# Optimization experiments

Hardware: AMD Instinct MI355X
Metric: run time of the kernel (lower is better)

Reference implementation:

```python
import jax, jax.numpy as jnp
import numpy as np

N = 10000      # nodes
E = 160000     # edges
IN = 256       # input feature dim
HID = 128      # hidden per head
H = 4          # heads (all layers)
EMB = 128      # dim_embedding (last-layer out per head)
SLOPE = 0.2    # leaky_relu negative slope in attention


def _gat_layer(h, src, dst, W, al, ar, b, residual, apply_act):
    """DGL-style GATConv (no dropout). h: [N, F_in], W: [F_in, H*D], al/ar/b: [H, D]."""
    n = h.shape[0]
    heads, d = al.shape
    feat = (h @ W).reshape(n, heads, d)                 # [N, H, D]
    el = jnp.sum(feat * al, axis=-1)                    # [N, H]
    er = jnp.sum(feat * ar, axis=-1)                    # [N, H]
    e = jax.nn.leaky_relu(el[src] + er[dst], SLOPE)     # [E, H]
    # edge softmax over incoming edges of dst (numerically stable)
    m = jax.ops.segment_max(e, dst, num_segments=n)
    m = jnp.where(jnp.isfinite(m), m, 0.0)              # empty segments -> 0
    ex = jnp.exp(e - m[dst])
    den = jax.ops.segment_sum(ex, dst, num_segments=n)
    alpha = ex / jnp.maximum(den[dst], 1e-9)            # [E, H]
    rst = jax.ops.segment_sum(alpha[:, :, None] * feat[src], dst, num_segments=n)  # [N, H, D]
    if residual:
        rst = rst + h.reshape(n, heads, d)              # identity residual (dims match)
    rst = rst + b
    return jax.nn.elu(rst) if apply_act else rst


def setup_inputs() -> dict:
    key = jax.random.key(0)
    ks = jax.random.split(key, 24)
    def p(k, shape, scale):
        return (jax.random.normal(k, shape, jnp.float32) * scale)
    inp = {
        'x': jax.random.normal(ks[0], (N, IN), jnp.float32),
        'src': jax.random.randint(ks[1], (E,), 0, N, dtype=jnp.int32).astype(jnp.int64),
        'dst': jax.random.randint(ks[2], (E,), 0, N, dtype=jnp.int32).astype(jnp.int64),
        # layer 0: in=IN, out=HID per head
        'W0': p(ks[3], (IN, H * HID), 1.0 / np.sqrt(IN)),
        'al0': p(ks[4], (H, HID), 0.1), 'ar0': p(ks[5], (H, HID), 0.1),
        'b0': p(ks[6], (H, HID), 0.02),
        # layer 1: in=H*HID=512, out=HID per head, residual
        'W1': p(ks[7], (H * HID, H * HID), 1.0 / np.sqrt(H * HID)),
        'al1': p(ks[8], (H, HID), 0.1), 'ar1': p(ks[9], (H, HID), 0.1),
        'b1': p(ks[10], (H, HID), 0.02),
        # layer 2: in=H*HID=512, out=EMB per head, residual, no activation
        'W2': p(ks[11], (H * HID, H * EMB), 1.0 / np.sqrt(H * HID)),
        'al2': p(ks[12], (H, EMB), 0.1), 'ar2': p(ks[13], (H, EMB), 0.1),
        'b2': p(ks[14], (H, EMB), 0.02),
        # MLP predictor: 2*EMB -> EMB -> EMB//2 -> 1
        'Wm0': p(ks[15], (2 * EMB, EMB), 1.0 / np.sqrt(2 * EMB)), 'bm0': p(ks[16], (EMB,), 0.02),
        'Wm1': p(ks[17], (EMB, EMB // 2), 1.0 / np.sqrt(EMB)), 'bm1': p(ks[18], (EMB // 2,), 0.02),
        'Wm2': p(ks[19], (EMB // 2, 1), 1.0 / np.sqrt(EMB // 2)), 'bm2': p(ks[20], (1,), 0.02),
    }
    return inp


def reference(x, src, dst, W0, al0, ar0, b0, W1, al1, ar1, b1, W2, al2, ar2, b2,
              Wm0, bm0, Wm1, bm1, Wm2, bm2):
    # GAT encoder
    h = _gat_layer(x, src, dst, W0, al0, ar0, b0, residual=False, apply_act=True).reshape(N, -1)
    h = _gat_layer(h, src, dst, W1, al1, ar1, b1, residual=True, apply_act=True).reshape(N, -1)
    h = _gat_layer(h, src, dst, W2, al2, ar2, b2, residual=True, apply_act=False).mean(axis=1)  # [N, EMB]
    # link predictor over all graph edges
    emb = jnp.concatenate([h[src], h[dst]], axis=1)     # [E, 2*EMB]
    z = jax.nn.relu(emb @ Wm0 + bm0)
    z = jax.nn.relu(z @ Wm1 + bm1)
    return jax.nn.sigmoid(z @ Wm2 + bm2)                # [E, 1]
```

## Files before the change

### kernel.cpp

```cpp
#include <hip/hip_runtime.h>
#include <hip/hip_bf16.h>
#include <math.h>

constexpr int kN = 10000;
constexpr int kE = 160000;
constexpr float kSlope = 0.2f;

typedef short v8s __attribute__((ext_vector_type(8)));
typedef float f32x4 __attribute__((ext_vector_type(4)));
typedef unsigned short ushort_t;

__device__ __forceinline__ float lrelu(float x) { return x > 0.f ? x : kSlope * x; }
__device__ __forceinline__ float elu_f(float x) { return x > 0.f ? x : (expf(x) - 1.f); }
__device__ __forceinline__ float b2f(ushort_t u) {
    return __uint_as_float(((unsigned)u) << 16);
}
__device__ __forceinline__ ushort_t f2b(float f) {
    unsigned u = __float_as_uint(f);
    return (ushort_t)((u + 0x7FFFu + ((u >> 16) & 1u)) >> 16);
}

__global__ void detect_zero(const void* __restrict__ x, const void* __restrict__ dsti,
                            int* __restrict__ flags, int* __restrict__ deg) {
    if (blockIdx.x == 0) {
        __shared__ int sb[2];
        int tid = threadIdx.x;
        if (tid == 0) { sb[0] = 0; sb[1] = 0; }
        __syncthreads();
        const ushort_t* xb = (const ushort_t*)x;
        int big = 0;
        for (int i = tid; i < 4096; i += 256) {
            float v = b2f(xb[i]);
            if (!(fabsf(v) <= 1e4f)) big = 1;
        }
        const int* d32 = (const int*)dsti;
        int hi = 0;
        for (int i = tid; i < 4096; i += 256) hi |= d32[2 * i + 1];
        if (big) atomicOr(&sb[0], 1);
        if (hi)  atomicOr(&sb[1], 1);
        __syncthreads();
        if (tid == 0) { flags[0] = sb[0]; flags[1] = sb[1] ? 0 : 1; }
    } else {
        int i = (blockIdx.x - 1) * 256 + threadIdx.x;
        if (i < 2 * kN) deg[i] = 0;
    }
}

struct PrepArgs {
    const void* sm[13];
    const void* W0; const void* W1; const void* W2; const void* Wm0; const void* Wm1;
    const void* X; const void* srcIn; const void* dstIn;
    float* smallb;
    ushort_t* W0T; ushort_t* W1T; ushort_t* W2T; ushort_t* PQT; ushort_t* Wm1T;
    ushort_t* Xb;
    int* nsrc; int* ndst; int* deg;
    const int* flags;
};
constexpr int kPrepTotal = 4865 + 131072 + 262144 + 262144 + 32768 + 8192 + 2560000 + 320000;

__global__ void prep_all(PrepArgs a) {
    int i = blockIdx.x * 256 + threadIdx.x;
    if (i >= kPrepTotal) return;
    const int f32in = a.flags[0];
    auto cv = [&](const void* p, int idx) -> ushort_t {
        return f32in ? f2b(((const float*)p)[idx]) : ((const ushort_t*)p)[idx];
    };
    if (i < 4865) {
        int seg, offi;
        if (i < 4608)      { seg = i >> 9; offi = i & 511; }
        else if (i < 4736) { seg = 9;  offi = i - 4608; }
        else if (i < 4800) { seg = 10; offi = i - 4736; }
        else if (i < 4864) { seg = 11; offi = i - 4800; }
        else               { seg = 12; offi = 0; }
        a.smallb[i] = f32in ? ((const float*)a.sm[seg])[offi]
                            : b2f(((const ushort_t*)a.sm[seg])[offi]);
        return;
    }
    i -= 4865;
    if (i < 131072) {
        int n = i >> 8, k = i & 255;
        a.W0T[i] = cv(a.W0, k * 512 + n);
        return;
    }
    i -= 131072;
    if (i < 262144) {
        int n = i >> 9, k = i & 511;
        a.W1T[i] = cv(a.W1, k * 512 + n);
        return;
    }
    i -= 262144;
    if (i < 262144) {
        int n = i >> 9, k = i & 511;
        a.W2T[i] = cv(a.W2, k * 512 + n);
        return;
    }
    i -= 262144;
    if (i < 32768) {
        int n = i >> 7, k = i & 127;
        a.PQT[i] = cv(a.Wm0, (k + ((n < 128) ? 0 : 128)) * 128 + (n & 127));
        return;
    }
    i -= 32768;
    if (i < 8192) {
        int n = i >> 7, k = i & 127;
        a.Wm1T[i] = cv(a.Wm1, k * 64 + n);
        return;
    }
    i -= 8192;
    if (i < 2560000) {
        if (f32in) a.Xb[i] = f2b(((const float*)a.X)[i]);
        return;
    }
    i -= 2560000;
    {
        const void* in = (i < kE) ? a.srcIn : a.dstIn;
        int j = (i < kE) ? i : i - kE;
        int v = a.flags[1] ? (int)((const long long*)in)[j] : ((const int*)in)[j];
        v = ((unsigned)v < (unsigned)kN) ? v : 0;
        if (i < kE) a.nsrc[j] = v;
        else { a.ndst[j] = v; atomicAdd(&a.deg[v], 1); }
    }
}

__global__ __launch_bounds__(1024) void scan_off(const int* __restrict__ deg,
                                                 int* __restrict__ off, int n) {
    __shared__ int s[1024];
    int tid = threadIdx.x;
    int per = (n + 1023) >> 10;
    int base = tid * per;
    int sum = 0;
    for (int i = 0; i < per; ++i) { int j = base + i; if (j < n) sum += deg[j]; }
    s[tid] = sum;
    __syncthreads();
    for (int d = 1; d < 1024; d <<= 1) {
        int v = (tid >= d) ? s[tid - d] : 0;
        __syncthreads();
        s[tid] += v;
        __syncthreads();
    }
    int run = (tid > 0) ? s[tid - 1] : 0;
    for (int i = 0; i < per; ++i) {
        int j = base + i;
        if (j < n) { off[j] = run; run += deg[j]; }
    }
    if (tid == 0) off[n] = s[1023];
}

__global__ void fill_csr(const int* __restrict__ src, const int* __restrict__ dst,
                         const int* __restrict__ off, int* __restrict__ cnt,
                         int* __restrict__ ss, int* __restrict__ eid,
                         int* __restrict__ dpos, int n) {
    int i = blockIdx.x * 256 + threadIdx.x;
    if (i < n) {
        int d = dst[i];
        int pos = off[d] + atomicAdd(&cnt[d], 1);
        if (pos < kE) { ss[pos] = src[i]; eid[pos] = i; dpos[pos] = d; }
    }
}

template <bool ELER>
__global__ __launch_bounds__(256) void gemm_mfma(const ushort_t* __restrict__ A,
                                                 const void* __restrict__ Araw,
                                                 const int* __restrict__ gflags,
                                                 const ushort_t* __restrict__ WT,
                                                 ushort_t* __restrict__ Cout,
                                                 int M, int N, int K,
                                                 const float* __restrict__ al,
                                                 const float* __restrict__ ar,
                                                 float* __restrict__ el,
                                                 float* __restrict__ er) {
    __shared__ __align__(16) ushort_t As[4][64][8];
    __shared__ __align__(16) ushort_t Bs[4][128][8];
    __shared__ float elred[64][2][2];
    const int t = threadIdx.x;
    const int wave = t >> 6, lane = t & 63;
    const int l16 = lane & 15, q = lane >> 4;
    const int row0 = blockIdx.y * 64, col0 = blockIdx.x * 128;
    const int wm = (wave & 1) * 32, wn = (wave >> 1) * 64;
    const int am = t >> 2, ak8 = t & 3;
    const int sw = ak8 * 4;

    const ushort_t* Aeff = A;
    if (Araw != nullptr && gflags[0] == 0) Aeff = (const ushort_t*)Araw;

    const ushort_t* aptr = Aeff + (size_t)min(row0 + am, M - 1) * K + ak8 * 8;
    const ushort_t* bptr0 = WT + (size_t)(col0 + am) * K + ak8 * 8;
    const ushort_t* bptr1 = bptr0 + (size_t)64 * K;

    uint4 ga  = *(const uint4*)aptr;
    uint4 gb0 = *(const uint4*)bptr0;
    uint4 gb1 = *(const uint4*)bptr1;

    f32x4 acc[2][4];
#pragma unroll
    for (int mt = 0; mt < 2; ++mt)
#pragma unroll
        for (int nt = 0; nt < 4; ++nt)
#pragma unroll
            for (int r = 0; r < 4; ++r) acc[mt][nt][r] = 0.f;

    for (int k0 = 0; k0 < K; k0 += 32) {
        __syncthreads();
        *(uint4*)&As[ak8][am ^ sw][0] = ga;
        *(uint4*)&Bs[ak8][am ^ sw][0] = gb0;
        *(uint4*)&Bs[ak8][(am + 64) ^ sw][0] = gb1;
        __syncthreads();
        if (k0 + 32 < K) {
            ga  = *(const uint4*)(aptr + k0 + 32);
            gb0 = *(const uint4*)(bptr0 + k0 + 32);
            gb1 = *(const uint4*)(bptr1 + k0 + 32);
        }
        v8s af[2], bf[4];
        const int qs = q * 4;
#pragma unroll
        for (int mt = 0; mt < 2; ++mt)
            af[mt] = *(const v8s*)&As[q][(wm + mt * 16 + l16) ^ qs][0];
#pragma unroll
        for (int nt = 0; nt < 4; ++nt)
            bf[nt] = *(const v8s*)&Bs[q][(wn + nt * 16 + l16) ^ qs][0];
#pragma unroll
        for (int mt = 0; mt < 2; ++mt)
#pragma unroll
            for (int nt = 0; nt < 4; ++nt)
                acc[mt][nt] = __builtin_amdgcn_mfma_f32_16x16x32_bf16(af[mt], bf[nt],
                                                                      acc[mt][nt], 0, 0, 0);
    }
#pragma unroll
    for (int mt = 0; mt < 2; ++mt)
#pragma unroll
        for (int r = 0; r < 4; ++r) {
            int row = row0 + wm + mt * 16 + q * 4 + r;
            if (row < M) {
#pragma unroll
                for (int nt = 0; nt < 4; ++nt)
                    Cout[(size_t)row * N + col0 + wn + nt * 16 + l16] = f2b(acc[mt][nt][r]);
            }
        }
    if (ELER) {
        const int head = blockIdx.x;
        float alv[4], arv[4];
#pragma unroll
        for (int nt = 0; nt < 4; ++nt) {
            alv[nt] = al[head * 128 + wn + nt * 16 + l16];
            arv[nt] = ar[head * 128 + wn + nt * 16 + l16];
        }
#pragma unroll
        for (int mt = 0; mt < 2; ++mt)
#pragma unroll
            for (int r = 0; r < 4; ++r) {
                float pel = 0.f, per = 0.f;
#pragma unroll
                for (int nt = 0; nt < 4; ++nt) {
                    pel += acc[mt][nt][r] * alv[nt];
                    per += acc[mt][nt][r] * arv[nt];
                }
                pel += __shfl_xor(pel, 1); per += __shfl_xor(per, 1);
                pel += __shfl_xor(pel, 2); per += __shfl_xor(per, 2);
                pel += __shfl_xor(pel, 4); per += __shfl_xor(per, 4);
                pel += __shfl_xor(pel, 8); per += __shfl_xor(per, 8);
                if (l16 == 0) {
                    int rl = wm + mt * 16 + q * 4 + r;
                    elred[rl][wave >> 1][0] = pel;
                    elred[rl][wave >> 1][1] = per;
                }
            }
        __syncthreads();
        if (t < 64) {
            int row = row0 + t;
            if (row < M) {
                el[row * 4 + head] = elred[t][0][0] + elred[t][1][0];
                er[row * 4 + head] = elred[t][0][1] + elred[t][1][1];
            }
        }
    }
}

template <bool RES, bool ACT, int EPI>
__global__ __launch_bounds__(256) void gat_agg(const ushort_t* __restrict__ feat,
                                               const float* __restrict__ el,
                                               const float* __restrict__ er,
                                               const int* __restrict__ off,
                                               const int* __restrict__ ss,
                                               const ushort_t* residb,
                                               const float* __restrict__ bias,
                                               ushort_t* hl) {
    const int node = blockIdx.x * 4 + (threadIdx.x >> 6);
    const int lane = threadIdx.x & 63;
    if (node >= kN) return;
    const int off0 = off[node];
    const int deg = off[node + 1] - off0;
    float4 er4 = *(const float4*)(er + node * 4);
    const int head = lane >> 4;
    const float erh = (head == 0) ? er4.x : (head == 1) ? er4.y : (head == 2) ? er4.z : er4.w;

    const int c0 = lane * 8;
    float den = 0.f;
    float acc0[8] = {};
    float acc1[8] = {};
    if (deg > 0) {
        int sA = ss[off0];
        int sB = (deg > 1) ? ss[off0 + 1] : sA;
        float eA = el[sA * 4 + head];
        float eB = el[sB * 4 + head];
        const ushort_t* fA = feat + (size_t)sA * 512 + c0;
        const ushort_t* fB = feat + (size_t)sB * 512 + c0;
        ushort4 a0 = *(const ushort4*)fA, a1 = *(const ushort4*)(fA + 4);
        ushort4 b0 = *(const ushort4*)fB, b1 = *(const ushort4*)(fB + 4);
        for (int j = 0; j < deg; j += 2) {
            int sC = (j + 2 < deg) ? ss[off0 + j + 2] : sA;
            int sD = (j + 3 < deg) ? ss[off0 + j + 3] : sA;
            float eC = el[sC * 4 + head];
            float eD = el[sD * 4 + head];
            const ushort_t* fC = feat + (size_t)sC * 512 + c0;
            const ushort_t* fD = feat + (size_t)sD * 512 + c0;
            ushort4 c0v = *(const ushort4*)fC, c1v = *(const ushort4*)(fC + 4);
            ushort4 d0v = *(const ushort4*)fD, d1v = *(const ushort4*)(fD + 4);
            {
                float w0 = expf(lrelu(eA + erh));
                den += w0;
                acc0[0] += w0 * b2f(a0.x); acc0[1] += w0 * b2f(a0.y);
                acc0[2] += w0 * b2f(a0.z); acc0[3] += w0 * b2f(a0.w);
                acc0[4] += w0 * b2f(a1.x); acc0[5] += w0 * b2f(a1.y);
                acc0[6] += w0 * b2f(a1.z); acc0[7] += w0 * b2f(a1.w);
            }
            if (j + 1 < deg) {
                float w1 = expf(lrelu(eB + erh));
                den += w1;
                acc1[0] += w1 * b2f(b0.x); acc1[1] += w1 * b2f(b0.y);
                acc1[2] += w1 * b2f(b0.z); acc1[3] += w1 * b2f(b0.w);
                acc1[4] += w1 * b2f(b1.x); acc1[5] += w1 * b2f(b1.y);
                acc1[6] += w1 * b2f(b1.z); acc1[7] += w1 * b2f(b1.w);
            }
            eA = eC; eB = eD;
            a0 = c0v; a1 = c1v; b0 = d0v; b1 = d1v;
        }
    }
    const float inv = 1.f / fmaxf(den, 1e-9f);
    float4 b0 = *(const float4*)(bias + c0);
    float4 b1 = *(const float4*)(bias + c0 + 4);
    float v[8];
#pragma unroll
    for (int r = 0; r < 8; ++r) v[r] = (acc0[r] + acc1[r]) * inv;
    v[0] += b0.x; v[1] += b0.y; v[2] += b0.z; v[3] += b0.w;
    v[4] += b1.x; v[5] += b1.y; v[6] += b1.z; v[7] += b1.w;
    if (RES) {
        const ushort_t* rp = residb + (size_t)node * 512 + c0;
        ushort4 r0 = *(const ushort4*)rp;
        ushort4 r1 = *(const ushort4*)(rp + 4);
        v[0] += b2f(r0.x); v[1] += b2f(r0.y); v[2] += b2f(r0.z); v[3] += b2f(r0.w);
        v[4] += b2f(r1.x); v[5] += b2f(r1.y); v[6] += b2f(r1.z); v[7] += b2f(r1.w);
    }
    if (ACT) {
#pragma unroll
        for (int r = 0; r < 8; ++r) v[r] = elu_f(v[r]);
    }
    if (EPI == 1) {
        ushort_t* hp = hl + (size_t)node * 512 + c0;
        ushort4 h0 = {f2b(v[0]), f2b(v[1]), f2b(v[2]), f2b(v[3])};
        ushort4 h1 = {f2b(v[4]), f2b(v[5]), f2b(v[6]), f2b(v[7])};
        *(ushort4*)hp = h0;
        *(ushort4*)(hp + 4) = h1;
    }
    if (EPI == 2) {
        float m[8];
#pragma unroll
        for (int r = 0; r < 8; ++r) {
            float x = v[r] + __shfl_xor(v[r], 16);
            x += __shfl_xor(x, 32);
            m[r] = 0.25f * x;
        }
        if (lane < 16) {
            ushort_t* hp = hl + (size_t)node * 128 + lane * 8;
            ushort4 h0 = {f2b(m[0]), f2b(m[1]), f2b(m[2]), f2b(m[3])};
            ushort4 h1 = {f2b(m[4]), f2b(m[5]), f2b(m[6]), f2b(m[7])};
            *(ushort4*)hp = h0;
            *(ushort4*)(hp + 4) = h1;
        }
    }
}

__global__ __launch_bounds__(256) void edge_mfma(const ushort_t* __restrict__ PQb,
                                                 const float* __restrict__ bm0f,
                                                 const ushort_t* __restrict__ Wm1T,
                                                 const float* __restrict__ bm1f,
                                                 const float* __restrict__ wm2f,
                                                 const float* __restrict__ bm2f,
                                                 const int* __restrict__ ss,
                                                 const int* __restrict__ dpos,
                                                 const int* __restrict__ eid,
                                                 void* __restrict__ outv,
                                                 const int* __restrict__ flags) {
    const int t = threadIdx.x;
    const int wave = t >> 6, lane = t & 63;
    const int l16 = lane & 15, q = lane >> 4;
    const int base = blockIdx.x * 64 + wave * 16;
    const int pos = base + l16;
    const int s = ss[pos], d = dpos[pos];
    const ushort_t* prow = PQb + (size_t)s * 256;
    const ushort_t* qrow = PQb + (size_t)d * 256 + 128;

    f32x4 acc[4];
#pragma unroll
    for (int nt = 0; nt < 4; ++nt)
#pragma unroll
        for (int r = 0; r < 4; ++r) acc[nt][r] = 0.f;

#pragma unroll
    for (int ks = 0; ks < 4; ++ks) {
        const int k0 = ks * 32 + q * 8;
        ushort4 p0 = *(const ushort4*)(prow + k0);
        ushort4 p1 = *(const ushort4*)(prow + k0 + 4);
        ushort4 q0 = *(const ushort4*)(qrow + k0);
        ushort4 q1 = *(const ushort4*)(qrow + k0 + 4);
        float4 bb0 = *(const float4*)(bm0f + k0);
        float4 bb1 = *(const float4*)(bm0f + k0 + 4);
        v8s a;
        a[0] = (short)f2b(fmaxf(b2f(p0.x) + b2f(q0.x) + bb0.x, 0.f));
        a[1] = (short)f2b(fmaxf(b2f(p0.y) + b2f(q0.y) + bb0.y, 0.f));
        a[2] = (short)f2b(fmaxf(b2f(p0.z) + b2f(q0.z) + bb0.z, 0.f));
        a[3] = (short)f2b(fmaxf(b2f(p0.w) + b2f(q0.w) + bb0.w, 0.f));
        a[4] = (short)f2b(fmaxf(b2f(p1.x) + b2f(q1.x) + bb1.x, 0.f));
        a[5] = (short)f2b(fmaxf(b2f(p1.y) + b2f(q1.y) + bb1.y, 0.f));
        a[6] = (short)f2b(fmaxf(b2f(p1.z) + b2f(q1.z) + bb1.z, 0.f));
        a[7] = (short)f2b(fmaxf(b2f(p1.w) + b2f(q1.w) + bb1.w, 0.f));
#pragma unroll
        for (int nt = 0; nt < 4; ++nt) {
            v8s b = *(const v8s*)(Wm1T + (size_t)(nt * 16 + l16) * 128 + k0);
            acc[nt] = __builtin_amdgcn_mfma_f32_16x16x32_bf16(a, b, acc[nt], 0, 0, 0);
        }
    }
    float b1v[4], w2v[4];
#pragma unroll
    for (int nt = 0; nt < 4; ++nt) {
        b1v[nt] = bm1f[nt * 16 + l16];
        w2v[nt] = wm2f[nt * 16 + l16];
    }
    float b2 = bm2f[0];
    const int f32out = flags[0];
#pragma unroll
    for (int r = 0; r < 4; ++r) {
        float v = 0.f;
#pragma unroll
        for (int nt = 0; nt < 4; ++nt)
            v += fmaxf(acc[nt][r] + b1v[nt], 0.f) * w2v[nt];
        v += __shfl_xor(v, 1);
        v += __shfl_xor(v, 2);
        v += __shfl_xor(v, 4);
        v += __shfl_xor(v, 8);
        if (l16 == 0) {
            int e = eid[base + q * 4 + r];
            float rr = 1.f / (1.f + expf(-(v + b2)));
            if (f32out) ((float*)outv)[e] = rr;
            else        ((ushort_t*)outv)[e] = f2b(rr);
        }
    }
}

extern "C" void kernel_launch(void* const* d_in, const int* in_sizes, int n_in,
                              void* d_out, int out_size, void* d_ws, size_t ws_size,
                              hipStream_t stream) {
    (void)in_sizes; (void)n_in; (void)out_size; (void)ws_size;

    float* w = (float*)d_ws;
    size_t o = 0;
    auto alloc = [&](size_t n) { float* p = w + o; o += (n + 3) & ~size_t(3); return p; };
    float* smallb = alloc(4868);
    float* al0f = smallb + 0;    float* ar0f = smallb + 512;  float* b0f  = smallb + 1024;
    float* al1f = smallb + 1536; float* ar1f = smallb + 2048; float* b1f  = smallb + 2560;
    float* al2f = smallb + 3072; float* ar2f = smallb + 3584; float* b2f_ = smallb + 4096;
    float* bm0f = smallb + 4608; float* bm1f = smallb + 4736;
    float* wm2f = smallb + 4800; float* bm2f = smallb + 4864;
    float* elb  = alloc((size_t)kN * 4);
    float* erb  = alloc((size_t)kN * 4);
    ushort_t* Fb  = (ushort_t*)alloc((size_t)kN * 256);
    ushort_t* AHL = (ushort_t*)alloc((size_t)kN * 256);
    ushort_t* MHb = (ushort_t*)alloc((size_t)kN * 64);
    ushort_t* Xb  = (ushort_t*)alloc((size_t)kN * 128);
    ushort_t* W0T  = (ushort_t*)alloc(65536);
    ushort_t* W1T  = (ushort_t*)alloc(131072);
    ushort_t* W2T  = (ushort_t*)alloc(131072);
    ushort_t* PQT  = (ushort_t*)alloc(16384);
    ushort_t* Wm1T = (ushort_t*)alloc(4096);
    int* ip    = (int*)(w + o);
    int* flags = ip;
    int* deg   = ip + 4;
    int* cnt   = deg + kN;
    int* off   = cnt + kN;
    int* ss    = off + 10004;
    int* eid   = ss + kE;
    int* dpos  = eid + kE;
    int* nsrc  = dpos + kE;
    int* ndst  = nsrc + kE;

    ushort_t* PQb = Fb;

    dim3 blk(256);

    detect_zero<<<dim3(1 + (2 * kN + 255) / 256), blk, 0, stream>>>(d_in[0], d_in[2], flags, deg);

    PrepArgs a;
    const int sidx[13] = {4, 5, 6, 8, 9, 10, 12, 13, 14, 16, 18, 19, 20};
    for (int i = 0; i < 13; ++i) a.sm[i] = d_in[sidx[i]];
    a.W0 = d_in[3]; a.W1 = d_in[7]; a.W2 = d_in[11]; a.Wm0 = d_in[15]; a.Wm1 = d_in[17];
    a.X = d_in[0]; a.srcIn = d_in[1]; a.dstIn = d_in[2];
    a.smallb = smallb; a.W0T = W0T; a.W1T = W1T; a.W2T = W2T; a.PQT = PQT; a.Wm1T = Wm1T;
    a.Xb = Xb; a.nsrc = nsrc; a.ndst = ndst; a.deg = deg; a.flags = flags;
    prep_all<<<dim3((kPrepTotal + 255) / 256), blk, 0, stream>>>(a);

    scan_off<<<dim3(1), dim3(1024), 0, stream>>>(deg, off, kN);
    fill_csr<<<dim3((kE + 255) / 256), blk, 0, stream>>>(nsrc, ndst, off, cnt, ss, eid, dpos, kE);

    const int gy = (kN + 63) / 64;
    const int ga = (kN + 3) / 4;

    gemm_mfma<true><<<dim3(4, gy), blk, 0, stream>>>(Xb, d_in[0], flags, W0T, Fb,
                                                     kN, 512, 256, al0f, ar0f, elb, erb);
    gat_agg<false, true, 1><<<dim3(ga), blk, 0, stream>>>(Fb, elb, erb, off, ss,
                                                          nullptr, b0f, AHL);

    gemm_mfma<true><<<dim3(4, gy), blk, 0, stream>>>(AHL, nullptr, flags, W1T, Fb,
                                                     kN, 512, 512, al1f, ar1f, elb, erb);
    gat_agg<true, true, 1><<<dim3(ga), blk, 0, stream>>>(Fb, elb, erb, off, ss,
                                                         AHL, b1f, AHL);

    gemm_mfma<true><<<dim3(4, gy), blk, 0, stream>>>(AHL, nullptr, flags, W2T, Fb,
                                                     kN, 512, 512, al2f, ar2f, elb, erb);
    gat_agg<true, false, 2><<<dim3(ga), blk, 0, stream>>>(Fb, elb, erb, off, ss,
                                                          AHL, b2f_, MHb);

    gemm_mfma<false><<<dim3(2, gy), blk, 0, stream>>>(MHb, nullptr, flags, PQT, PQb,
                                                      kN, 256, 128,
                                                      nullptr, nullptr, nullptr, nullptr);

    edge_mfma<<<dim3(kE / 64), blk, 0, stream>>>(PQb, bm0f, Wm1T, bm1f, wm2f, bm2f,
                                                 ss, dpos, eid, d_out, flags);
}
```

Baseline: 326.0 us.

## Double-buffer GEMM via direct global-to-LDS loads and deepen aggregation prefetch

The GEMM now stages tiles with global_load_lds directly into a double-buffered shared-memory layout. This removes the register round trip and one barrier per K step, so loads for the next tile overlap with MFMA work. The aggregation kernel prefetches four neighbours at a time using 16-byte loads and single accumulators, and uses fast __expf. The link-predictor loads are widened to uint4. The risks are a possible LDS swizzle or layout mismatch with the direct-to-LDS writes, and fast-math exp precision differences.

```diff
diff --git a/kernel.cpp b/kernel.cpp
--- a/kernel.cpp
+++ b/kernel.cpp
@@ -11,13 +11,20 @@
 typedef unsigned short ushort_t;
 
 __device__ __forceinline__ float lrelu(float x) { return x > 0.f ? x : kSlope * x; }
-__device__ __forceinline__ float elu_f(float x) { return x > 0.f ? x : (expf(x) - 1.f); }
+__device__ __forceinline__ float elu_f(float x) { return x > 0.f ? x : (__expf(x) - 1.f); }
 __device__ __forceinline__ float b2f(ushort_t u) {
     return __uint_as_float(((unsigned)u) << 16);
 }
+__device__ __forceinline__ float bl(unsigned u) { return __uint_as_float(u << 16); }
+__device__ __forceinline__ float bh(unsigned u) { return __uint_as_float(u & 0xffff0000u); }
 __device__ __forceinline__ ushort_t f2b(float f) {
     unsigned u = __float_as_uint(f);
     return (ushort_t)((u + 0x7FFFu + ((u >> 16) & 1u)) >> 16);
+}
+__device__ __forceinline__ void gload16(const void* g, void* l) {
+    __builtin_amdgcn_global_load_lds(
+        (const __attribute__((address_space(1))) void*)g,
+        (__attribute__((address_space(3))) void*)l, 16, 0, 0);
 }
 
 __global__ void detect_zero(const void* __restrict__ x, const void* __restrict__ dsti,
@@ -169,27 +176,28 @@
                                                  const float* __restrict__ ar,
                                                  float* __restrict__ el,
                                                  float* __restrict__ er) {
-    __shared__ __align__(16) ushort_t As[4][64][8];
-    __shared__ __align__(16) ushort_t Bs[4][128][8];
+    __shared__ __align__(16) ushort_t As[2][4][64][8];
+    __shared__ __align__(16) ushort_t Bs[2][4][128][8];
     __shared__ float elred[64][2][2];
     const int t = threadIdx.x;
     const int wave = t >> 6, lane = t & 63;
     const int l16 = lane & 15, q = lane >> 4;
     const int row0 = blockIdx.y * 64, col0 = blockIdx.x * 128;
     const int wm = (wave & 1) * 32, wn = (wave >> 1) * 64;
-    const int am = t >> 2, ak8 = t & 3;
-    const int sw = ak8 * 4;
 
     const ushort_t* Aeff = A;
     if (Araw != nullptr && gflags[0] == 0) Aeff = (const ushort_t*)Araw;
 
-    const ushort_t* aptr = Aeff + (size_t)min(row0 + am, M - 1) * K + ak8 * 8;
-    const ushort_t* bptr0 = WT + (size_t)(col0 + am) * K + ak8 * 8;
-    const ushort_t* bptr1 = bptr0 + (size_t)64 * K;
-
-    uint4 ga  = *(const uint4*)aptr;
-    uint4 gb0 = *(const uint4*)bptr0;
-    uint4 gb1 = *(const uint4*)bptr1;
+    const int lsw = lane ^ (wave * 4);
+    const ushort_t* asrc  = Aeff + (size_t)min(row0 + lsw, M - 1) * K + wave * 8;
+    const ushort_t* bsrc0 = WT + (size_t)(col0 + lsw) * K + wave * 8;
+    const ushort_t* bsrc1 = WT + (size_t)(col0 + 64 + lsw) * K + wave * 8;
+
+    auto stage = [&](int b, int k0) {
+        gload16(asrc + k0,  &As[b][wave][0][0]);
+        gload16(bsrc0 + k0, &Bs[b][wave][0][0]);
+        gload16(bsrc1 + k0, &Bs[b][wave][64][0]);
+    };
 
     f32x4 acc[2][4];
 #pragma unroll
@@ -199,32 +207,34 @@
 #pragma unroll
             for (int r = 0; r < 4; ++r) acc[mt][nt][r] = 0.f;
 
-    for (int k0 = 0; k0 < K; k0 += 32) {
-        __syncthreads();
-        *(uint4*)&As[ak8][am ^ sw][0] = ga;
-        *(uint4*)&Bs[ak8][am ^ sw][0] = gb0;
-        *(uint4*)&Bs[ak8][(am + 64) ^ sw][0] = gb1;
-        __syncthreads();
-        if (k0 + 32 < K) {
-            ga  = *(const uint4*)(aptr + k0 + 32);
-            gb0 = *(const uint4*)(bptr0 + k0 + 32);
-            gb1 = *(const uint4*)(bptr1 + k0 + 32);
-        }
+    const int qs = q * 4;
+    auto compute = [&](int b) {
         v8s af[2], bf[4];
-        const int qs = q * 4;
 #pragma unroll
         for (int mt = 0; mt < 2; ++mt)
-            af[mt] = *(const v8s*)&As[q][(wm + mt * 16 + l16) ^ qs][0];
+            af[mt] = *(const v8s*)&As[b][q][(wm + mt * 16 + l16) ^ qs][0];
 #pragma unroll
         for (int nt = 0; nt < 4; ++nt)
-            bf[nt] = *(const v8s*)&Bs[q][(wn + nt * 16 + l16) ^ qs][0];
+            bf[nt] = *(const v8s*)&Bs[b][q][(wn + nt * 16 + l16) ^ qs][0];
 #pragma unroll
         for (int mt = 0; mt < 2; ++mt)
 #pragma unroll
             for (int nt = 0; nt < 4; ++nt)
                 acc[mt][nt] = __builtin_amdgcn_mfma_f32_16x16x32_bf16(af[mt], bf[nt],
                                                                       acc[mt][nt], 0, 0, 0);
-    }
+    };
+
+    stage(0, 0);
+    __syncthreads();
+    for (int k0 = 0; k0 < K; k0 += 64) {
+        stage(1, k0 + 32);
+        compute(0);
+        __syncthreads();
+        if (k0 + 64 < K) stage(0, k0 + 64);
+        compute(1);
+        __syncthreads();
+    }
+
 #pragma unroll
     for (int mt = 0; mt < 2; ++mt)
 #pragma unroll
@@ -292,47 +302,41 @@
     float4 er4 = *(const float4*)(er + node * 4);
     const int head = lane >> 4;
     const float erh = (head == 0) ? er4.x : (head == 1) ? er4.y : (head == 2) ? er4.z : er4.w;
-
     const int c0 = lane * 8;
+
     float den = 0.f;
-    float acc0[8] = {};
-    float acc1[8] = {};
+    float acc[8] = {};
     if (deg > 0) {
-        int sA = ss[off0];
-        int sB = (deg > 1) ? ss[off0 + 1] : sA;
-        float eA = el[sA * 4 + head];
-        float eB = el[sB * 4 + head];
-        const ushort_t* fA = feat + (size_t)sA * 512 + c0;
-        const ushort_t* fB = feat + (size_t)sB * 512 + c0;
-        ushort4 a0 = *(const ushort4*)fA, a1 = *(const ushort4*)(fA + 4);
-        ushort4 b0 = *(const ushort4*)fB, b1 = *(const ushort4*)(fB + 4);
-        for (int j = 0; j < deg; j += 2) {
-            int sC = (j + 2 < deg) ? ss[off0 + j + 2] : sA;
-            int sD = (j + 3 < deg) ? ss[off0 + j + 3] : sA;
-            float eC = el[sC * 4 + head];
-            float eD = el[sD * 4 + head];
-            const ushort_t* fC = feat + (size_t)sC * 512 + c0;
-            const ushort_t* fD = feat + (size_t)sD * 512 + c0;
-            ushort4 c0v = *(const ushort4*)fC, c1v = *(const ushort4*)(fC + 4);
-            ushort4 d0v = *(const ushort4*)fD, d1v = *(const ushort4*)(fD + 4);
-            {
-                float w0 = expf(lrelu(eA + erh));
-                den += w0;
-                acc0[0] += w0 * b2f(a0.x); acc0[1] += w0 * b2f(a0.y);
-                acc0[2] += w0 * b2f(a0.z); acc0[3] += w0 * b2f(a0.w);
-                acc0[4] += w0 * b2f(a1.x); acc0[5] += w0 * b2f(a1.y);
-                acc0[6] += w0 * b2f(a1.z); acc0[7] += w0 * b2f(a1.w);
+        float eP[4]; uint4 fP[4];
+#pragma unroll
+        for (int i = 0; i < 4; ++i) {
+            int s = ss[off0 + min(i, deg - 1)];
+            eP[i] = el[s * 4 + head];
+            fP[i] = *(const uint4*)(feat + (size_t)s * 512 + c0);
+        }
+        for (int j = 0; j < deg; j += 4) {
+            float eN[4]; uint4 fN[4];
+            if (j + 4 < deg) {
+#pragma unroll
+                for (int i = 0; i < 4; ++i) {
+                    int s = ss[off0 + min(j + 4 + i, deg - 1)];
+                    eN[i] = el[s * 4 + head];
+                    fN[i] = *(const uint4*)(feat + (size_t)s * 512 + c0);
+                }
             }
-            if (j + 1 < deg) {
-                float w1 = expf(lrelu(eB + erh));
-                den += w1;
-                acc1[0] += w1 * b2f(b0.x); acc1[1] += w1 * b2f(b0.y);
-                acc1[2] += w1 * b2f(b0.z); acc1[3] += w1 * b2f(b0.w);
-                acc1[4] += w1 * b2f(b1.x); acc1[5] += w1 * b2f(b1.y);
-                acc1[6] += w1 * b2f(b1.z); acc1[7] += w1 * b2f(b1.w);
+#pragma unroll
+            for (int i = 0; i < 4; ++i) {
+                if (j + i < deg) {
+                    float w = __expf(lrelu(eP[i] + erh));
+                    den += w;
+                    acc[0] += w * bl(fP[i].x); acc[1] += w * bh(fP[i].x);
+                    acc[2] += w * bl(fP[i].y); acc[3] += w * bh(fP[i].y);
+                    acc[4] += w * bl(fP[i].z); acc[5] += w * bh(fP[i].z);
+                    acc[6] += w * bl(fP[i].w); acc[7] += w * bh(fP[i].w);
+                }
             }
-            eA = eC; eB = eD;
-            a0 = c0v; a1 = c1v; b0 = d0v; b1 = d1v;
+#pragma unroll
+            for (int i = 0; i < 4; ++i) { eP[i] = eN[i]; fP[i] = fN[i]; }
         }
     }
     const float inv = 1.f / fmaxf(den, 1e-9f);
@@ -340,15 +344,15 @@
     float4 b1 = *(const float4*)(bias + c0 + 4);
     float v[8];
 #pragma unroll
-    for (int r = 0; r < 8; ++r) v[r] = (acc0[r] + acc1[r]) * inv;
+    for (int r = 0; r < 8; ++r) v[r] = acc[r] * inv;
     v[0] += b0.x; v[1] += b0.y; v[2] += b0.z; v[3] += b0.w;
     v[4] += b1.x; v[5] += b1.y; v[6] += b1.z; v[7] += b1.w;
     if (RES) {
-        const ushort_t* rp = residb + (size_t)node * 512 + c0;
-        ushort4 r0 = *(const ushort4*)rp;
-        ushort4 r1 = *(const ushort4*)(rp + 4);
-        v[0] += b2f(r0.x); v[1] += b2f(r0.y); v[2] += b2f(r0.z); v[3] += b2f(r0.w);
-        v[4] += b2f(r1.x); v[5] += b2f(r1.y); v[6] += b2f(r1.z); v[7] += b2f(r1.w);
+        uint4 rv = *(const uint4*)(residb + (size_t)node * 512 + c0);
+        v[0] += bl(rv.x); v[1] += bh(rv.x);
+        v[2] += bl(rv.y); v[3] += bh(rv.y);
+        v[4] += bl(rv.z); v[5] += bh(rv.z);
+        v[6] += bl(rv.w); v[7] += bh(rv.w);
     }
     if (ACT) {
 #pragma unroll
@@ -408,21 +412,19 @@
 #pragma unroll
     for (int ks = 0; ks < 4; ++ks) {
         const int k0 = ks * 32 + q * 8;
-        ushort4 p0 = *(const ushort4*)(prow + k0);
-        ushort4 p1 = *(const ushort4*)(prow + k0 + 4);
-        ushort4 q0 = *(const ushort4*)(qrow + k0);
-        ushort4 q1 = *(const ushort4*)(qrow + k0 + 4);
+        uint4 pv = *(const uint4*)(prow + k0);
+        uint4 qv = *(const uint4*)(qrow + k0);
         float4 bb0 = *(const float4*)(bm0f + k0);
         float4 bb1 = *(const float4*)(bm0f + k0 + 4);
         v8s a;
-        a[0] = (short)f2b(fmaxf(b2f(p0.x) + b2f(q0.x) + bb0.x, 0.f));
-        a[1] = (short)f2b(fmaxf(b2f(p0.y) + b2f(q0.y) + bb0.y, 0.f));
-        a[2] = (short)f2b(fmaxf(b2f(p0.z) + b2f(q0.z) + bb0.z, 0.f));
-        a[3] = (short)f2b(fmaxf(b2f(p0.w) + b2f(q0.w) + bb0.w, 0.f));
-        a[4] = (short)f2b(fmaxf(b2f(p1.x) + b2f(q1.x) + bb1.x, 0.f));
-        a[5] = (short)f2b(fmaxf(b2f(p1.y) + b2f(q1.y) + bb1.y, 0.f));
-        a[6] = (short)f2b(fmaxf(b2f(p1.z) + b2f(q1.z) + bb1.z, 0.f));
-        a[7] = (short)f2b(fmaxf(b2f(p1.w) + b2f(q1.w) + bb1.w, 0.f));
+        a[0] = (short)f2b(fmaxf(bl(pv.x) + bl(qv.x) + bb0.x, 0.f));
+        a[1] = (short)f2b(fmaxf(bh(pv.x) + bh(qv.x) + bb0.y, 0.f));
+        a[2] = (short)f2b(fmaxf(bl(pv.y) + bl(qv.y) + bb0.z, 0.f));
+        a[3] = (short)f2b(fmaxf(bh(pv.y) + bh(qv.y) + bb0.w, 0.f));
+        a[4] = (short)f2b(fmaxf(bl(pv.z) + bl(qv.z) + bb1.x, 0.f));
+        a[5] = (short)f2b(fmaxf(bh(pv.z) + bh(qv.z) + bb1.y, 0.f));
+        a[6] = (short)f2b(fmaxf(bl(pv.w) + bl(qv.w) + bb1.z, 0.f));
+        a[7] = (short)f2b(fmaxf(bh(pv.w) + bh(qv.w) + bb1.w, 0.f));
 #pragma unroll
         for (int nt = 0; nt < 4; ++nt) {
             v8s b = *(const v8s*)(Wm1T + (size_t)(nt * 16 + l16) * 128 + k0);
@@ -449,7 +451,7 @@
         v += __shfl_xor(v, 8);
         if (l16 == 0) {
             int e = eid[base + q * 4 + r];
-            float rr = 1.f / (1.f + expf(-(v + b2)));
+            float rr = 1.f / (1.f + __expf(-(v + b2)));
             if (f32out) ((float*)outv)[e] = rr;
             else        ((ushort_t*)outv)[e] = f2b(rr);
         }
```

New measurement: 335.6 us. +2.9%, slower.
